# Performance work log

Measured on AMD Instinct MI355X. Metric: run time of the kernel, lower is better.

The kernel has to match this reference:

```python
import jax, jax.numpy as jnp
import numpy as np

L, P = 8, 512
HID = 128
N_COARSE, N_FINE = 64, 128
LVIS_NEAR, LVIS_FAR = 1e-3, 0.5
S = 100.0  # 1 / fixed_s_recp


def _mlp_sdf(x, w0, b0, w1, b1, w2, b2, w3, b3):
    # x: [..., 3] -> sdf [...]
    h = jax.nn.relu(x @ w0 + b0)
    h = jax.nn.relu(h @ w1 + b1)
    h = jax.nn.relu(h @ w2 + b2)
    return (h @ w3 + b3)[..., 0]


def _sdf_to_w(sdf, s):
    # faithful to sdf_to_w: cdf -> alpha -> visibility weights via cumprod
    cdf = jax.nn.sigmoid(sdf * s)
    alpha = jnp.clip((cdf[..., :-1] - cdf[..., 1:]) / (cdf[..., :-1] + 1e-10), 0.0, None)
    ones = jnp.ones(alpha.shape[:-1] + (1,), alpha.dtype)
    shifted = jnp.concatenate([ones, 1.0 - alpha + 1e-10], axis=-1)
    return alpha * jnp.cumprod(shifted, axis=-1)[..., :-1]


def _sample_pdf(bins, weights, u):
    # standard NeRF importance sampling; bins [...,M+1], weights [...,M], u [...,N]
    weights = weights + 1e-5
    pdf = weights / jnp.sum(weights, axis=-1, keepdims=True)
    cdf = jnp.cumsum(pdf, axis=-1)
    cdf = jnp.concatenate([jnp.zeros_like(cdf[..., :1]), cdf], axis=-1)  # [...,M+1]
    # searchsorted (right) via broadcast compare: [...,N,M+1]
    inds = jnp.sum((u[..., None] >= cdf[..., None, :]).astype(jnp.int32), axis=-1)
    below = jnp.clip(inds - 1, 0, cdf.shape[-1] - 1)
    above = jnp.clip(inds, 0, cdf.shape[-1] - 1)
    cdf_b = jnp.take_along_axis(cdf, below, axis=-1)
    cdf_a = jnp.take_along_axis(cdf, above, axis=-1)
    bins_b = jnp.take_along_axis(bins, below, axis=-1)
    bins_a = jnp.take_along_axis(bins, above, axis=-1)
    denom = cdf_a - cdf_b
    denom = jnp.where(denom < 1e-5, jnp.ones_like(denom), denom)
    t = (u - cdf_b) / denom
    return bins_b + t * (bins_a - bins_b)


def setup_inputs() -> dict:
    key = jax.random.key(0)
    ks = jax.random.split(key, 8)

    def lin(k, fi, fo):
        return jax.random.normal(k, (fi, fo), jnp.float32) / jnp.sqrt(jnp.float32(fi))

    return {
        "pts": jax.random.normal(ks[0], (1, P, 3), jnp.float32) * 0.5,
        "light_posi": jax.random.normal(ks[1], (L, 3), jnp.float32) * 2.0,
        "u": jax.random.uniform(ks[2], (L, P, N_FINE), jnp.float32),
        "w0": lin(ks[3], 3, HID), "b0": jnp.zeros((HID,), jnp.float32),
        "w1": lin(ks[4], HID, HID), "b1": jnp.zeros((HID,), jnp.float32),
        "w2": lin(ks[5], HID, HID), "b2": jnp.zeros((HID,), jnp.float32),
        "w3": lin(ks[6], HID, 1), "b3": jnp.zeros((1,), jnp.float32),
    }


def reference(pts, light_posi, u, w0, b0, w1, b1, w2, b2, w3, b3):
    sdf = lambda x: _mlp_sdf(x, w0, b0, w1, b1, w2, b2, w3, b3)
    # pts: [1,P,3]; light_posi: [L,3]
    pts2l = light_posi[:, None, :] - pts  # [L,P,3]
    pts2l = pts2l / jnp.linalg.norm(pts2l, axis=-1, keepdims=True)
    t = jnp.linspace(0.0, 1.0 - 1.0 / N_COARSE, N_COARSE, dtype=jnp.float32)
    d_coarse = LVIS_NEAR * (1.0 - t) + LVIS_FAR * t  # [N_COARSE]
    d_coarse = jnp.broadcast_to(d_coarse, (pts2l.shape[0], pts.shape[1], N_COARSE))
    # coarse sample points: [L,P,Nc,3]
    pts_coarse = pts[:, :, None, :] + d_coarse[..., None] * pts2l[:, :, None, :]
    w_coarse = _sdf_to_w(sdf(pts_coarse), S)  # [L,P,Nc-1]
    d_fine = _sample_pdf(d_coarse, w_coarse, u)  # [L,P,Nf]
    d_all = jnp.sort(jnp.concatenate([d_coarse, d_fine], axis=-1), axis=-1)  # [L,P,Nc+Nf]
    pts_all = pts[:, :, None, :] + d_all[..., None] * pts2l[:, :, None, :]
    w_all = _sdf_to_w(sdf(pts_all), S)
    occu = jnp.sum(w_all, axis=-1)  # [L,P]
    return 1.0 - occu
```

## Files before the change

kernel.cpp:

```cpp
#include <hip/hip_runtime.h>
#include <math.h>

#define NL 8
#define NP 512
#define NC 64
#define NF 128
#define NALL 192
#define NRAY (NL * NP)
#define HID 128

typedef _Float16 half8 __attribute__((ext_vector_type(8)));
typedef _Float16 half4v __attribute__((ext_vector_type(4)));
typedef float floatx16 __attribute__((ext_vector_type(16)));
typedef unsigned long long ull;

#define MFMA(a, b, c) __builtin_amdgcn_mfma_f32_32x32x16_f16((a), (b), (c), 0, 0, 0)


__device__ __forceinline__ float dcoarse_at(int i) {
    float t = (float)i * 0.015625f;
    return 1e-3f * (1.0f - t) + 0.5f * t;
}

__device__ __forceinline__ floatx16 fzero16() {
    floatx16 z;
#pragma unroll
    for (int i = 0; i < 16; ++i) z[i] = 0.f;
    return z;
}
__device__ __forceinline__ half8 hzero8() {
    half8 z;
#pragma unroll
    for (int i = 0; i < 8; ++i) z[i] = (_Float16)0.f;
    return z;
}

__global__ void prep_kernel(const float* __restrict__ w1, const float* __restrict__ w2,
                            _Float16* __restrict__ Wsp) {
    int f = blockIdx.x * 256 + threadIdx.x;
    int layer = blockIdx.y;
    const float* w = layer ? w2 : w1;
    int i = f & 7, l31 = (f >> 3) & 31, lhi = (f >> 8) & 1, ks = (f >> 9) & 7, jb = f >> 12;
    int j = jb * 32 + l31;
    int k = ks * 16 + lhi * 8 + i;
    float v = w[k * 128 + j];
    _Float16 hi = (_Float16)v;
    Wsp[(layer * 2 + 0) * 16384 + f] = hi;
    Wsp[(layer * 2 + 1) * 16384 + f] = (_Float16)(v - (float)hi);
}

template<int MODE, int FASTW>
__global__ __launch_bounds__(256, 4) void mlp_kernel(
    const float* __restrict__ pts, const float* __restrict__ lights,
    const float* __restrict__ d_fine,
    const float* __restrict__ w0, const float* __restrict__ b0,
    const float* __restrict__ w1, const float* __restrict__ b1,
    const float* __restrict__ w2, const float* __restrict__ b2,
    const float* __restrict__ w3, const float* __restrict__ b3,
    const _Float16* __restrict__ Wsp,
    float* __restrict__ sdf_out)
{
    __shared__ __align__(16) _Float16 Hhi[64 * 128];
    __shared__ __align__(16) _Float16 Hlo[64 * 128];
    __shared__ _Float16 Xs[6 * 64];
    __shared__ float P2[2 * 64];

    const int tid = threadIdx.x;
    const int lane = tid & 63;
    const int wv = tid >> 6;
    const int jh = wv & 1, mh = wv >> 1;
    const int l31 = lane & 31, lhi = lane >> 5;
    const int base = blockIdx.x * 64;

    if (tid < 64) {
        int pt = base + tid;
        int ray; float d;
        if (MODE == 0) { ray = pt >> 6; d = dcoarse_at(pt & 63); }
        else           { ray = pt >> 7; d = d_fine[pt]; }
        int l = ray >> 9, p = ray & (NP - 1);
        float px = pts[p * 3 + 0], py = pts[p * 3 + 1], pz = pts[p * 3 + 2];
        float dx = lights[l * 3 + 0] - px, dy = lights[l * 3 + 1] - py, dz = lights[l * 3 + 2] - pz;
        float n = sqrtf(dx * dx + dy * dy + dz * dz);
        dx /= n; dy /= n; dz /= n;
        float xc[3] = { px + d * dx, py + d * dy, pz + d * dz };
#pragma unroll
        for (int c = 0; c < 3; ++c) {
            _Float16 h = (_Float16)xc[c];
            Xs[c * 64 + tid] = h;
            Xs[(3 + c) * 64 + tid] = (_Float16)(xc[c] - (float)h);
        }
    }
    __syncthreads();

    const int m0 = mh * 32;

    auto haddr = [&](int m, int k0) {
        return m * 128 + ((((k0 >> 3) ^ (m & 15)) << 3) | (k0 & 7));
    };

    auto store_tile = [&](const floatx16& a, int jt, const float* __restrict__ bias) {
        int m = m0 + l31;
#pragma unroll
        for (int g = 0; g < 4; ++g) {
            int jg = jh * 64 + jt * 32 + 8 * g + 4 * lhi;
            half4v hq, lq;
#pragma unroll
            for (int q = 0; q < 4; ++q) {
                float v = fmaxf(a[g * 4 + q] + bias[jg + q], 0.f);
                _Float16 hi = (_Float16)v;
                hq[q] = hi;
                lq[q] = (_Float16)(v - (float)hi);
            }
            int ad = haddr(m, jg);
            *(half4v*)&Hhi[ad] = hq;
            *(half4v*)&Hlo[ad] = lq;
        }
    };

    floatx16 acc[2];

    {
        half8 a1h[2], a1l[2], bh1, bl1;
#pragma unroll
        for (int jt = 0; jt < 2; ++jt) { a1h[jt] = hzero8(); a1l[jt] = hzero8(); }
        bh1 = hzero8(); bl1 = hzero8();
        if (lhi == 0) {
#pragma unroll
            for (int jt = 0; jt < 2; ++jt) {
                int j = jh * 64 + jt * 32 + l31;
#pragma unroll
                for (int c = 0; c < 3; ++c) {
                    float v = w0[c * 128 + j];
                    _Float16 hi = (_Float16)v;
                    a1h[jt][c] = hi;
                    a1l[jt][c] = (_Float16)(v - (float)hi);
                }
            }
            int m = m0 + l31;
#pragma unroll
            for (int c = 0; c < 3; ++c) {
                bh1[c] = Xs[c * 64 + m];
                bl1[c] = Xs[(3 + c) * 64 + m];
            }
        }
#pragma unroll
        for (int jt = 0; jt < 2; ++jt) acc[jt] = fzero16();
#pragma unroll
        for (int jt = 0; jt < 2; ++jt) acc[jt] = MFMA(a1l[jt], bh1, acc[jt]);
#pragma unroll
        for (int jt = 0; jt < 2; ++jt) acc[jt] = MFMA(a1h[jt], bl1, acc[jt]);
#pragma unroll
        for (int jt = 0; jt < 2; ++jt) acc[jt] = MFMA(a1h[jt], bh1, acc[jt]);
#pragma unroll
        for (int jt = 0; jt < 2; ++jt) store_tile(acc[jt], jt, b0);
    }
    __syncthreads();

    auto ldA = [&](int L, int jt, int ks, half8& ah, half8& al) {
        if (FASTW) {
            int off = ((((jh * 2 + jt) * 8 + ks) * 2 + lhi) * 32 + l31) * 8;
            ah = *(const half8*)&Wsp[(L * 2 + 0) * 16384 + off];
            al = *(const half8*)&Wsp[(L * 2 + 1) * 16384 + off];
        } else {
            const float* w = L ? w2 : w1;
            int j = jh * 64 + jt * 32 + l31, k0 = ks * 16 + lhi * 8;
#pragma unroll
            for (int i = 0; i < 8; ++i) {
                float v = w[(k0 + i) * 128 + j];
                _Float16 hi = (_Float16)v;
                ah[i] = hi;
                al[i] = (_Float16)(v - (float)hi);
            }
        }
    };

    auto gemm = [&](int L) {
        const int m = m0 + l31;
#pragma unroll
        for (int jt = 0; jt < 2; ++jt) acc[jt] = fzero16();
#pragma unroll
        for (int ks = 0; ks < 8; ++ks) {
            int ad = haddr(m, ks * 16 + lhi * 8);
            half8 bh = *(const half8*)&Hhi[ad];
            half8 bl = *(const half8*)&Hlo[ad];
            half8 ah[2], al[2];
            ldA(L, 0, ks, ah[0], al[0]);
            ldA(L, 1, ks, ah[1], al[1]);
            acc[0] = MFMA(al[0], bh, acc[0]);
            acc[1] = MFMA(al[1], bh, acc[1]);
            acc[0] = MFMA(ah[0], bl, acc[0]);
            acc[1] = MFMA(ah[1], bl, acc[1]);
            acc[0] = MFMA(ah[0], bh, acc[0]);
            acc[1] = MFMA(ah[1], bh, acc[1]);
        }
    };

    gemm(0);
    __syncthreads();
#pragma unroll
    for (int jt = 0; jt < 2; ++jt) store_tile(acc[jt], jt, b1);
    __syncthreads();

    gemm(1);
    {
        float p = 0.f;
#pragma unroll
        for (int jt = 0; jt < 2; ++jt)
#pragma unroll
            for (int g = 0; g < 4; ++g) {
                int jg = jh * 64 + jt * 32 + 8 * g + 4 * lhi;
#pragma unroll
                for (int q = 0; q < 4; ++q) {
                    float v = fmaxf(acc[jt][g * 4 + q] + b2[jg + q], 0.f);
                    p = fmaf(v, w3[jg + q], p);
                }
            }
        p += __shfl_xor(p, 32);
        if (lane < 32) P2[jh * 64 + m0 + l31] = p;
    }
    __syncthreads();
    if (tid < 64) sdf_out[base + tid] = b3[0] + P2[tid] + P2[64 + tid];
}

__global__ __launch_bounds__(256) void sample_kernel(
    const float* __restrict__ sdf_c, const float* __restrict__ u,
    float* __restrict__ d_fine, unsigned char* __restrict__ perm8) {
    const int lane = threadIdx.x & 63, wv = threadIdx.x >> 6;
    const int ray = blockIdx.x * 4 + wv;

    float sv = sdf_c[ray * NC + lane];
    float c = 1.0f / (1.0f + expf(-100.0f * sv));
    float cn = __shfl_down(c, 1);
    bool valid = lane < 63;
    float a = valid ? fmaxf((c - cn) / (c + 1e-10f), 0.f) : 0.f;
    float sh = valid ? (1.f - a + 1e-10f) : 1.f;
    float ps = sh;
#pragma unroll
    for (int off = 1; off < 64; off <<= 1) { float o = __shfl_up(ps, off); if (lane >= off) ps *= o; }
    float T = __shfl_up(ps, 1);
    if (lane == 0) T = 1.f;
    float w = valid ? (a * T + 1e-5f) : 0.f;
    float wsum = w;
#pragma unroll
    for (int off = 1; off < 64; off <<= 1) wsum += __shfl_xor(wsum, off);
    float pdf = w / wsum;
    float cs = pdf;
#pragma unroll
    for (int off = 1; off < 64; off <<= 1) { float o = __shfl_up(cs, off); if (lane >= off) cs += o; }
    float cdfv = __shfl_up(cs, 1);
    if (lane == 0) cdfv = 0.f;

    float df[2];
#pragma unroll
    for (int t = 0; t < 2; ++t) {
        float uu = u[ray * NF + t * 64 + lane];
        int lo = 0;
#pragma unroll
        for (int b = 32; b >= 1; b >>= 1) {
            float cm = __shfl(cdfv, lo + b);
            if (uu >= cm) lo += b;
        }
        int above = min(lo + 1, NC - 1);
        float cb = __shfl(cdfv, lo), ca = __shfl(cdfv, above);
        float bb = dcoarse_at(lo), ba = dcoarse_at(above);
        float denom = ca - cb;
        if (denom < 1e-5f) denom = 1.f;
        float tt = (uu - cb) / denom;
        df[t] = bb + tt * (ba - bb);
        d_fine[ray * 128 + t * 64 + lane] = df[t];
    }

    ull v[4];
    v[0] = ((ull)__float_as_uint(dcoarse_at(lane)) << 32) | (unsigned)lane;
    v[1] = ((ull)__float_as_uint(df[0]) << 32) | (unsigned)(64 + lane);
    v[2] = ((ull)__float_as_uint(df[1]) << 32) | (unsigned)(128 + lane);
    v[3] = ((ull)0x7F800000u << 32) | 255u;
    for (int k = 2; k <= 256; k <<= 1) {
        for (int j = k >> 1; j > 0; j >>= 1) {
            if (j >= 64) {
                int tj = j >> 6;
#pragma unroll
                for (int t = 0; t < 4; ++t) {
                    if ((t & tj) == 0) {
                        int t2 = t ^ tj;
                        bool asc = (((t * 64) & k) == 0);
                        ull x = v[t], y = v[t2];
                        bool sw = asc ? (x > y) : (x < y);
                        if (sw) { v[t] = y; v[t2] = x; }
                    }
                }
            } else {
#pragma unroll
                for (int t = 0; t < 4; ++t) {
                    int i = t * 64 + lane;
                    ull other = __shfl_xor(v[t], j);
                    bool lower = (lane & j) == 0;
                    bool asc = ((i & k) == 0);
                    bool takeMin = (lower == asc);
                    ull mn = v[t] < other ? v[t] : other;
                    ull mx = v[t] < other ? other : v[t];
                    v[t] = takeMin ? mn : mx;
                }
            }
        }
    }
#pragma unroll
    for (int t = 0; t < 3; ++t)
        perm8[ray * NALL + t * 64 + lane] = (unsigned char)(v[t] & 0xFFu);
}

__global__ __launch_bounds__(256) void finish_kernel(
    const float* __restrict__ sdf_c, const float* __restrict__ sdf_f,
    const unsigned char* __restrict__ perm8, float* __restrict__ out) {
    int lane = threadIdx.x & 63, wv = threadIdx.x >> 6;
    int ray = blockIdx.x * 4 + wv;
    const unsigned char* P = perm8 + (size_t)ray * NALL;
    float c[4];
#pragma unroll
    for (int t = 0; t < 4; ++t) {
        int i = lane * 3 + t;
        if (i < NALL) {
            int idx = P[i];
            float s = (idx < 64) ? sdf_c[ray * NC + idx] : sdf_f[ray * 128 + (idx - 64)];
            c[t] = 1.0f / (1.0f + expf(-100.0f * s));
        } else c[t] = 0.f;
    }
    float a[3], s[3];
#pragma unroll
    for (int t = 0; t < 3; ++t) {
        int i = lane * 3 + t;
        if (i < NALL - 1) {
            a[t] = fmaxf((c[t] - c[t + 1]) / (c[t] + 1e-10f), 0.f);
            s[t] = 1.f - a[t] + 1e-10f;
        } else { a[t] = 0.f; s[t] = 1.f; }
    }
    float chunk = s[0] * s[1] * s[2];
    float ps = chunk;
#pragma unroll
    for (int off = 1; off < 64; off <<= 1) {
        float o = __shfl_up(ps, off);
        if (lane >= off) ps *= o;
    }
    float T = __shfl_up(ps, 1);
    if (lane == 0) T = 1.f;
    float occ = a[0] * T;
    T *= s[0]; occ = fmaf(a[1], T, occ);
    T *= s[1]; occ = fmaf(a[2], T, occ);
#pragma unroll
    for (int off = 1; off < 64; off <<= 1) occ += __shfl_xor(occ, off);
    if (lane == 0) out[ray] = 1.f - occ;
}

extern "C" void kernel_launch(void* const* d_in, const int* in_sizes, int n_in,
                              void* d_out, int out_size, void* d_ws, size_t ws_size,
                              hipStream_t stream) {
    const float* pts = (const float*)d_in[0];
    const float* lights = (const float*)d_in[1];
    const float* u = (const float*)d_in[2];
    const float* w0 = (const float*)d_in[3];
    const float* b0 = (const float*)d_in[4];
    const float* w1 = (const float*)d_in[5];
    const float* b1 = (const float*)d_in[6];
    const float* w2 = (const float*)d_in[7];
    const float* b2 = (const float*)d_in[8];
    const float* w3 = (const float*)d_in[9];
    const float* b3 = (const float*)d_in[10];
    float* out = (float*)d_out;

    char* wsb = (char*)d_ws;
    float* sdf_c = (float*)wsb;
    float* sdf_f = (float*)(wsb + (size_t)NRAY * NC * 4);
    float* d_fine = (float*)(wsb + (size_t)NRAY * (NC + 128) * 4);
    unsigned char* perm8 = (unsigned char*)(wsb + (size_t)NRAY * (NC + 256) * 4);
    _Float16* Wsp = (_Float16*)(wsb + (size_t)NRAY * (NC + 256) * 4 + (size_t)NRAY * NALL);
    const size_t need = (size_t)NRAY * (NC + 256) * 4 + (size_t)NRAY * NALL
                      + (size_t)4 * 16384 * sizeof(_Float16);
    const bool fast = ws_size >= need;

    if (fast) {
        prep_kernel<<<dim3(64, 2), 256, 0, stream>>>(w1, w2, Wsp);
        mlp_kernel<0, 1><<<(NRAY * NC) / 64, 256, 0, stream>>>(
            pts, lights, nullptr, w0, b0, w1, b1, w2, b2, w3, b3, Wsp, sdf_c);
        sample_kernel<<<NRAY / 4, 256, 0, stream>>>(sdf_c, u, d_fine, perm8);
        mlp_kernel<1, 1><<<(NRAY * 128) / 64, 256, 0, stream>>>(
            pts, lights, d_fine, w0, b0, w1, b1, w2, b2, w3, b3, Wsp, sdf_f);
    } else {
        mlp_kernel<0, 0><<<(NRAY * NC) / 64, 256, 0, stream>>>(
            pts, lights, nullptr, w0, b0, w1, b1, w2, b2, w3, b3, nullptr, sdf_c);
        sample_kernel<<<NRAY / 4, 256, 0, stream>>>(sdf_c, u, d_fine, perm8);
        mlp_kernel<1, 0><<<(NRAY * 128) / 64, 256, 0, stream>>>(
            pts, lights, d_fine, w0, b0, w1, b1, w2, b2, w3, b3, nullptr, sdf_f);
    }
    finish_kernel<<<NRAY / 4, 256, 0, stream>>>(sdf_c, sdf_f, perm8, out);
}
```

Baseline: 276.3 us.

## Enlarge MLP tile to 128 points with 8 waves and prefetch weight fragments

The SDF MLP kernel now processes 128 points per block with 512 threads. Each wave owns one 32-column slice of the output features and two 32-row point tiles, so every weight fragment loaded from global memory feeds two MFMAs instead of one. The first k-step weight fragment of each layer is loaded before the preceding barrier to hide its latency. Shared memory per block doubles to about 66KB and register pressure rises, which may cut how many blocks fit on a CU despite the launch bound of 4.

```diff
diff --git a/kernel.cpp b/kernel.cpp
--- a/kernel.cpp
+++ b/kernel.cpp
@@ -50,7 +50,7 @@
 }
 
 template<int MODE, int FASTW>
-__global__ __launch_bounds__(256, 4) void mlp_kernel(
+__global__ __launch_bounds__(512, 4) void mlp_kernel(
     const float* __restrict__ pts, const float* __restrict__ lights,
     const float* __restrict__ d_fine,
     const float* __restrict__ w0, const float* __restrict__ b0,
@@ -60,19 +60,19 @@
     const _Float16* __restrict__ Wsp,
     float* __restrict__ sdf_out)
 {
-    __shared__ __align__(16) _Float16 Hhi[64 * 128];
-    __shared__ __align__(16) _Float16 Hlo[64 * 128];
-    __shared__ _Float16 Xs[6 * 64];
-    __shared__ float P2[2 * 64];
+    __shared__ __align__(16) _Float16 Hhi[128 * 128];
+    __shared__ __align__(16) _Float16 Hlo[128 * 128];
+    __shared__ _Float16 Xs[6 * 128];
+    __shared__ float P2[4 * 128];
 
     const int tid = threadIdx.x;
     const int lane = tid & 63;
     const int wv = tid >> 6;
-    const int jh = wv & 1, mh = wv >> 1;
+    const int jq = wv & 3, mh = wv >> 2;
     const int l31 = lane & 31, lhi = lane >> 5;
-    const int base = blockIdx.x * 64;
-
-    if (tid < 64) {
+    const int base = blockIdx.x * 128;
+
+    if (tid < 128) {
         int pt = base + tid;
         int ray; float d;
         if (MODE == 0) { ray = pt >> 6; d = dcoarse_at(pt & 63); }
@@ -86,23 +86,23 @@
 #pragma unroll
         for (int c = 0; c < 3; ++c) {
             _Float16 h = (_Float16)xc[c];
-            Xs[c * 64 + tid] = h;
-            Xs[(3 + c) * 64 + tid] = (_Float16)(xc[c] - (float)h);
-        }
-    }
-    __syncthreads();
-
-    const int m0 = mh * 32;
+            Xs[c * 128 + tid] = h;
+            Xs[(3 + c) * 128 + tid] = (_Float16)(xc[c] - (float)h);
+        }
+    }
+    __syncthreads();
+
+    const int m0 = mh * 64;
 
     auto haddr = [&](int m, int k0) {
         return m * 128 + ((((k0 >> 3) ^ (m & 15)) << 3) | (k0 & 7));
     };
 
-    auto store_tile = [&](const floatx16& a, int jt, const float* __restrict__ bias) {
-        int m = m0 + l31;
+    auto store_tile = [&](const floatx16& a, int mt, const float* __restrict__ bias) {
+        int m = m0 + mt * 32 + l31;
 #pragma unroll
         for (int g = 0; g < 4; ++g) {
-            int jg = jh * 64 + jt * 32 + 8 * g + 4 * lhi;
+            int jg = jq * 32 + 8 * g + 4 * lhi;
             half4v hq, lq;
 #pragma unroll
             for (int q = 0; q < 4; ++q) {
@@ -119,51 +119,14 @@
 
     floatx16 acc[2];
 
-    {
-        half8 a1h[2], a1l[2], bh1, bl1;
-#pragma unroll
-        for (int jt = 0; jt < 2; ++jt) { a1h[jt] = hzero8(); a1l[jt] = hzero8(); }
-        bh1 = hzero8(); bl1 = hzero8();
-        if (lhi == 0) {
-#pragma unroll
-            for (int jt = 0; jt < 2; ++jt) {
-                int j = jh * 64 + jt * 32 + l31;
-#pragma unroll
-                for (int c = 0; c < 3; ++c) {
-                    float v = w0[c * 128 + j];
-                    _Float16 hi = (_Float16)v;
-                    a1h[jt][c] = hi;
-                    a1l[jt][c] = (_Float16)(v - (float)hi);
-                }
-            }
-            int m = m0 + l31;
-#pragma unroll
-            for (int c = 0; c < 3; ++c) {
-                bh1[c] = Xs[c * 64 + m];
-                bl1[c] = Xs[(3 + c) * 64 + m];
-            }
-        }
-#pragma unroll
-        for (int jt = 0; jt < 2; ++jt) acc[jt] = fzero16();
-#pragma unroll
-        for (int jt = 0; jt < 2; ++jt) acc[jt] = MFMA(a1l[jt], bh1, acc[jt]);
-#pragma unroll
-        for (int jt = 0; jt < 2; ++jt) acc[jt] = MFMA(a1h[jt], bl1, acc[jt]);
-#pragma unroll
-        for (int jt = 0; jt < 2; ++jt) acc[jt] = MFMA(a1h[jt], bh1, acc[jt]);
-#pragma unroll
-        for (int jt = 0; jt < 2; ++jt) store_tile(acc[jt], jt, b0);
-    }
-    __syncthreads();
-
-    auto ldA = [&](int L, int jt, int ks, half8& ah, half8& al) {
+    auto ldA = [&](int L, int ks, half8& ah, half8& al) {
         if (FASTW) {
-            int off = ((((jh * 2 + jt) * 8 + ks) * 2 + lhi) * 32 + l31) * 8;
+            int off = (((jq * 8 + ks) * 2 + lhi) * 32 + l31) * 8;
             ah = *(const half8*)&Wsp[(L * 2 + 0) * 16384 + off];
             al = *(const half8*)&Wsp[(L * 2 + 1) * 16384 + off];
         } else {
             const float* w = L ? w2 : w1;
-            int j = jh * 64 + jt * 32 + l31, k0 = ks * 16 + lhi * 8;
+            int j = jq * 32 + l31, k0 = ks * 16 + lhi * 8;
 #pragma unroll
             for (int i = 0; i < 8; ++i) {
                 float v = w[(k0 + i) * 128 + j];
@@ -174,52 +137,86 @@
         }
     };
 
-    auto gemm = [&](int L) {
-        const int m = m0 + l31;
-#pragma unroll
-        for (int jt = 0; jt < 2; ++jt) acc[jt] = fzero16();
+    {
+        half8 a1h = hzero8(), a1l = hzero8(), bh1[2], bl1[2];
+        bh1[0] = hzero8(); bh1[1] = hzero8(); bl1[0] = hzero8(); bl1[1] = hzero8();
+        if (lhi == 0) {
+            int j = jq * 32 + l31;
+#pragma unroll
+            for (int c = 0; c < 3; ++c) {
+                float v = w0[c * 128 + j];
+                _Float16 hi = (_Float16)v;
+                a1h[c] = hi;
+                a1l[c] = (_Float16)(v - (float)hi);
+            }
+#pragma unroll
+            for (int mt = 0; mt < 2; ++mt) {
+                int m = m0 + mt * 32 + l31;
+#pragma unroll
+                for (int c = 0; c < 3; ++c) {
+                    bh1[mt][c] = Xs[c * 128 + m];
+                    bl1[mt][c] = Xs[(3 + c) * 128 + m];
+                }
+            }
+        }
+        acc[0] = fzero16(); acc[1] = fzero16();
+        acc[0] = MFMA(a1l, bh1[0], acc[0]); acc[1] = MFMA(a1l, bh1[1], acc[1]);
+        acc[0] = MFMA(a1h, bl1[0], acc[0]); acc[1] = MFMA(a1h, bl1[1], acc[1]);
+        acc[0] = MFMA(a1h, bh1[0], acc[0]); acc[1] = MFMA(a1h, bh1[1], acc[1]);
+        store_tile(acc[0], 0, b0);
+        store_tile(acc[1], 1, b0);
+    }
+
+    auto gemm = [&](int L, half8 pa_h, half8 pa_l) {
+        acc[0] = fzero16(); acc[1] = fzero16();
 #pragma unroll
         for (int ks = 0; ks < 8; ++ks) {
-            int ad = haddr(m, ks * 16 + lhi * 8);
-            half8 bh = *(const half8*)&Hhi[ad];
-            half8 bl = *(const half8*)&Hlo[ad];
-            half8 ah[2], al[2];
-            ldA(L, 0, ks, ah[0], al[0]);
-            ldA(L, 1, ks, ah[1], al[1]);
-            acc[0] = MFMA(al[0], bh, acc[0]);
-            acc[1] = MFMA(al[1], bh, acc[1]);
-            acc[0] = MFMA(ah[0], bl, acc[0]);
-            acc[1] = MFMA(ah[1], bl, acc[1]);
-            acc[0] = MFMA(ah[0], bh, acc[0]);
-            acc[1] = MFMA(ah[1], bh, acc[1]);
+            half8 ah, al;
+            if (ks == 0) { ah = pa_h; al = pa_l; }
+            else         ldA(L, ks, ah, al);
+            half8 bh[2], bl[2];
+#pragma unroll
+            for (int mt = 0; mt < 2; ++mt) {
+                int ad = haddr(m0 + mt * 32 + l31, ks * 16 + lhi * 8);
+                bh[mt] = *(const half8*)&Hhi[ad];
+                bl[mt] = *(const half8*)&Hlo[ad];
+            }
+            acc[0] = MFMA(al, bh[0], acc[0]); acc[1] = MFMA(al, bh[1], acc[1]);
+            acc[0] = MFMA(ah, bl[0], acc[0]); acc[1] = MFMA(ah, bl[1], acc[1]);
+            acc[0] = MFMA(ah, bh[0], acc[0]); acc[1] = MFMA(ah, bh[1], acc[1]);
         }
     };
 
-    gemm(0);
-    __syncthreads();
-#pragma unroll
-    for (int jt = 0; jt < 2; ++jt) store_tile(acc[jt], jt, b1);
-    __syncthreads();
-
-    gemm(1);
-    {
+    half8 pfh, pfl;
+    ldA(0, 0, pfh, pfl);
+    __syncthreads();
+
+    gemm(0, pfh, pfl);
+    ldA(1, 0, pfh, pfl);
+    __syncthreads();
+    store_tile(acc[0], 0, b1);
+    store_tile(acc[1], 1, b1);
+    __syncthreads();
+
+    gemm(1, pfh, pfl);
+#pragma unroll
+    for (int mt = 0; mt < 2; ++mt) {
         float p = 0.f;
 #pragma unroll
-        for (int jt = 0; jt < 2; ++jt)
-#pragma unroll
-            for (int g = 0; g < 4; ++g) {
-                int jg = jh * 64 + jt * 32 + 8 * g + 4 * lhi;
-#pragma unroll
-                for (int q = 0; q < 4; ++q) {
-                    float v = fmaxf(acc[jt][g * 4 + q] + b2[jg + q], 0.f);
-                    p = fmaf(v, w3[jg + q], p);
-                }
-            }
+        for (int g = 0; g < 4; ++g) {
+            int jg = jq * 32 + 8 * g + 4 * lhi;
+#pragma unroll
+            for (int q = 0; q < 4; ++q) {
+                float v = fmaxf(acc[mt][g * 4 + q] + b2[jg + q], 0.f);
+                p = fmaf(v, w3[jg + q], p);
+            }
+        }
         p += __shfl_xor(p, 32);
-        if (lane < 32) P2[jh * 64 + m0 + l31] = p;
-    }
-    __syncthreads();
-    if (tid < 64) sdf_out[base + tid] = b3[0] + P2[tid] + P2[64 + tid];
+        if (lane < 32) P2[jq * 128 + m0 + mt * 32 + l31] = p;
+    }
+    __syncthreads();
+    if (tid < 128)
+        sdf_out[base + tid] = b3[0] + P2[tid] + P2[128 + tid] + P2[256 + tid] + P2[384 + tid];
 }
 
 __global__ __launch_bounds__(256) void sample_kernel(
@@ -379,16 +376,16 @@
 
     if (fast) {
         prep_kernel<<<dim3(64, 2), 256, 0, stream>>>(w1, w2, Wsp);
-        mlp_kernel<0, 1><<<(NRAY * NC) / 64, 256, 0, stream>>>(
+        mlp_kernel<0, 1><<<(NRAY * NC) / 128, 512, 0, stream>>>(
             pts, lights, nullptr, w0, b0, w1, b1, w2, b2, w3, b3, Wsp, sdf_c);
         sample_kernel<<<NRAY / 4, 256, 0, stream>>>(sdf_c, u, d_fine, perm8);
-        mlp_kernel<1, 1><<<(NRAY * 128) / 64, 256, 0, stream>>>(
+        mlp_kernel<1, 1><<<(NRAY * 128) / 128, 512, 0, stream>>>(
             pts, lights, d_fine, w0, b0, w1, b1, w2, b2, w3, b3, Wsp, sdf_f);
     } else {
-        mlp_kernel<0, 0><<<(NRAY * NC) / 64, 256, 0, stream>>>(
+        mlp_kernel<0, 0><<<(NRAY * NC) / 128, 512, 0, stream>>>(
             pts, lights, nullptr, w0, b0, w1, b1, w2, b2, w3, b3, nullptr, sdf_c);
         sample_kernel<<<NRAY / 4, 256, 0, stream>>>(sdf_c, u, d_fine, perm8);
-        mlp_kernel<1, 0><<<(NRAY * 128) / 64, 256, 0, stream>>>(
+        mlp_kernel<1, 0><<<(NRAY * 128) / 128, 512, 0, stream>>>(
             pts, lights, d_fine, w0, b0, w1, b1, w2, b2, w3, b3, nullptr, sdf_f);
     }
     finish_kernel<<<NRAY / 4, 256, 0, stream>>>(sdf_c, sdf_f, perm8, out);
```

Measured after the change: 241.4 us. 1.14x faster.
